# Optimization experiments

Measured on AMD Instinct MI355X. Metric: run time of the kernel, lower is better.

The kernel has to match this reference:

```python
import jax, jax.numpy as jnp
from jax import lax
import numpy as np

B, N = 64, 128           # graphs per batch, nodes per graph
MAX_LEVEL = 3
N_TRUNKS, TRUNK_LEN = 32, 32
H, OUT = 256, 10


def setup_inputs() -> dict:
    key = jax.random.key(0)
    ks = jax.random.split(key, 12)
    batch_feature = jax.random.normal(ks[0], (B, N), dtype=jnp.float32)
    trunk_idx = jax.random.randint(ks[1], (MAX_LEVEL, N_TRUNKS, TRUNK_LEN), 0, N, dtype=jnp.int32)
    trunk_len = jax.random.randint(ks[2], (MAX_LEVEL, N_TRUNKS), 1, TRUNK_LEN + 1, dtype=jnp.int32)
    s = 1.0 / np.sqrt(H)
    W_enc = jax.random.uniform(ks[3], (1, H), jnp.float32, -1.0, 1.0)
    b_enc = jax.random.uniform(ks[4], (H,), jnp.float32, -1.0, 1.0)
    W_ih = jax.random.uniform(ks[5], (MAX_LEVEL, 4 * H, H), jnp.float32, -s, s)
    W_hh = jax.random.uniform(ks[6], (MAX_LEVEL, 4 * H, H), jnp.float32, -s, s)
    b_ih = jax.random.uniform(ks[7], (MAX_LEVEL, 4 * H), jnp.float32, -s, s)
    b_hh = jax.random.uniform(ks[8], (MAX_LEVEL, 4 * H), jnp.float32, -s, s)
    W_lin = jax.random.uniform(ks[9], (MAX_LEVEL, H, OUT), jnp.float32, -s, s)
    b_lin = jax.random.uniform(ks[10], (MAX_LEVEL, OUT), jnp.float32, -s, s)
    return {"batch_feature": batch_feature, "trunk_idx": trunk_idx, "trunk_len": trunk_len,
            "W_enc": W_enc, "b_enc": b_enc, "W_ih": W_ih, "W_hh": W_hh,
            "b_ih": b_ih, "b_hh": b_hh, "W_lin": W_lin, "b_lin": b_lin}


def _lstm_scan(seq, W_ih, W_hh, b):
    """seq: [L, M, H] -> all hidden states [L, M, H] (single-layer LSTM, PyTorch gate order i,f,g,o)."""
    M = seq.shape[1]
    Hd = W_hh.shape[1]
    def step(carry, x_t):
        h, c = carry
        gates = x_t @ W_ih.T + h @ W_hh.T + b   # [M, 4H]
        i, f, g, o = jnp.split(gates, 4, axis=-1)
        c = jax.nn.sigmoid(f) * c + jax.nn.sigmoid(i) * jnp.tanh(g)
        h = jax.nn.sigmoid(o) * jnp.tanh(c)
        return (h, c), h
    init = (jnp.zeros((M, Hd), seq.dtype), jnp.zeros((M, Hd), seq.dtype))
    _, hs = lax.scan(step, init, seq)
    return hs


def reference(batch_feature, trunk_idx, trunk_len, W_enc, b_enc, W_ih, W_hh, b_ih, b_hh, W_lin, b_lin):
    Bv, Nv = batch_feature.shape
    Hd = W_enc.shape[1]
    # node encoder on scalar features: x [B*N, 1] @ W_enc [1, H]
    x_attr = (batch_feature.reshape(-1, 1) @ W_enc + b_enc).reshape(Bv, Nv, Hd)
    trunk_len = jnp.maximum(trunk_len, 1)
    score = jnp.zeros((Bv, W_lin.shape[-1]), x_attr.dtype)
    for l in range(trunk_idx.shape[0]):
        idx = trunk_idx[l]                       # [T, L]
        T, L = idx.shape
        seqs = x_attr[:, idx]                    # gather trunks -> [B, T, L, H]
        seqs = seqs.reshape(Bv * T, L, Hd).transpose(1, 0, 2)   # [L, B*T, H]
        hs = _lstm_scan(seqs, W_ih[l], W_hh[l], b_ih[l] + b_hh[l])  # [L, B*T, H]
        lens = jnp.tile(trunk_len[l], Bv)        # [B*T]
        h_last = hs[lens - 1, jnp.arange(Bv * T)]   # hidden at last valid step (== packed h_n)
        h_trunk = h_last.reshape(Bv, T, Hd).sum(axis=1)  # scatter-sum per graph (indices are i repeated T times)
        score = score + h_trunk @ W_lin[l] + b_lin[l]
    return score


if __name__ == "__main__":
    out = reference(**setup_inputs())
    print(out.shape, out.dtype)
```

## Files before the change

kernel.cpp:

```cpp
#include <hip/hip_runtime.h>
#include <hip/hip_bf16.h>
#include <stdint.h>

#define B_   64
#define N_   128
#define H_   256
#define FH   1024
#define NT   32
#define TL   32
#define LV   3
#define OUT_ 10
#define NTRK 96
#define UNITS 384

typedef __attribute__((ext_vector_type(4))) int   int4v;
typedef __attribute__((ext_vector_type(4))) float f32x4;

#define QW  (0.0625f / 127.0f)
#define QH  (1.0f / 127.0f)
#define QS  (QW * QH)
#define L2E 1.442695041f
#define QSI (-L2E * QS)
#define QSG (2.0f * L2E * QS)
#define C2  (2.0f * L2E)

__device__ inline float exp2f_(float x) { return __builtin_amdgcn_exp2f(x); }
__device__ inline float rcpf_(float x)  { return __builtin_amdgcn_rcpf(x); }

__global__ void prep_all(const float* __restrict__ W_enc, const float* __restrict__ b_enc,
                         const float* __restrict__ W_ih, const float* __restrict__ b_ih,
                         const float* __restrict__ b_hh, const float* __restrict__ W_hh,
                         const float* __restrict__ b_lin, const int* __restrict__ trunk_len,
                         float* __restrict__ u, float* __restrict__ v,
                         char* __restrict__ whh_i8, float* __restrict__ out,
                         int* __restrict__ sorted, int* __restrict__ counter) {
    int blk = blockIdx.x;
    int tid = threadIdx.x;
    if (blk < 768) {
        int j = blk * 4 + (tid >> 6);
        int lane = tid & 63;
        const float4 w  = ((const float4*)(W_ih + (size_t)j * H_))[lane];
        const float4 we = ((const float4*)W_enc)[lane];
        const float4 be = ((const float4*)b_enc)[lane];
        float du = w.x * we.x + w.y * we.y + w.z * we.z + w.w * we.w;
        float dv = w.x * be.x + w.y * be.y + w.z * be.z + w.w * be.w;
        for (int m = 32; m >= 1; m >>= 1) { du += __shfl_xor(du, m); dv += __shfl_xor(dv, m); }
        if (lane == 0) {
            int g = (j & 1023) >> 8;
            float s = (g == 2) ? (2.0f * L2E) : (-L2E);
            u[j] = s * du;
            v[j] = s * (dv + b_ih[j] + b_hh[j]);
        }
    } else if (blk < 1536) {
        int gid = (blk - 768) * 256 + tid;
        const float4 w = ((const float4*)W_hh)[gid];
        char4 o;
        int a0 = __float2int_rn(w.x * (127.0f / 0.0625f));
        int a1 = __float2int_rn(w.y * (127.0f / 0.0625f));
        int a2 = __float2int_rn(w.z * (127.0f / 0.0625f));
        int a3 = __float2int_rn(w.w * (127.0f / 0.0625f));
        a0 = a0 > 127 ? 127 : (a0 < -127 ? -127 : a0);
        a1 = a1 > 127 ? 127 : (a1 < -127 ? -127 : a1);
        a2 = a2 > 127 ? 127 : (a2 < -127 ? -127 : a2);
        a3 = a3 > 127 ? 127 : (a3 < -127 ? -127 : a3);
        o.x = (char)a0; o.y = (char)a1; o.z = (char)a2; o.w = (char)a3;
        ((char4*)whh_i8)[gid] = o;
        if (gid < B_ * OUT_) {
            int oo = gid % OUT_;
            out[gid] = b_lin[oo] + b_lin[OUT_ + oo] + b_lin[2 * OUT_ + oo];
        }
    } else {
        if (tid < NTRK) {
            int li = trunk_len[tid]; if (li < 1) li = 1;
            int rank = 0;
            for (int j2 = 0; j2 < NTRK; ++j2) {
                int lj = trunk_len[j2]; if (lj < 1) lj = 1;
                rank += (lj > li) || (lj == li && j2 < tid);
            }
            sorted[rank] = tid;
        }
        if (tid == 0) *counter = 0;
    }
}

__global__ __launch_bounds__(1024) __attribute__((amdgpu_waves_per_eu(4, 4)))
void lstm_main(const float* __restrict__ bfeat, const int* __restrict__ trunk_idx,
               const int* __restrict__ trunk_len,
               const char* __restrict__ whh_i8,
               const float* __restrict__ u, const float* __restrict__ v,
               const float* __restrict__ W_lin, const int* __restrict__ sorted,
               int* __restrict__ counter, float* __restrict__ out) {
    __shared__ __align__(16) char hbuf[2][16][272];
    __shared__ __align__(16) float sbuf[2][16];
    __shared__ int sh_uid;

    const int tid = threadIdx.x;
    const int w = tid >> 6;
    const int lane = tid & 63;
    const int col = lane & 15;
    const int q = lane >> 4;

    int4v z4; z4[0] = 0; z4[1] = 0; z4[2] = 0; z4[3] = 0;
    asm volatile("" : "+v"(z4));

    for (;;) {
        if (tid == 0) sh_uid = atomicAdd(counter, 1);
        __syncthreads();
        const int uid = sh_uid;
        if (uid >= UNITS) break;

        const int r = uid >> 2, qq = uid & 3;
        const int tt = sorted[r];
        const int l = tt >> 5;
        const int b0 = qq * 16;

        int len = trunk_len[tt];
        if (len < 1) len = 1;
        const int* tix = trunk_idx + tt * TL;
        const char* whh_l = whh_i8 + (size_t)l * FH * H_;

        int4v Breg[4][4];
        #pragma unroll
        for (int g = 0; g < 4; ++g) {
            int j = g * 256 + w * 16 + col;
            const char* bp = whh_l + (size_t)j * H_ + q * 16;
            #pragma unroll
            for (int k = 0; k < 4; ++k)
                Breg[g][k] = *(const int4v*)(bp + k * 64);
        }

        float u_r[4], v_r[4];
        {
            const float* u_l = u + l * FH;
            const float* v_l = v + l * FH;
            #pragma unroll
            for (int g = 0; g < 4; ++g) {
                int j = g * 256 + w * 16 + col;
                u_r[g] = u_l[j];
                v_r[g] = v_l[j];
            }
        }

        float c_r[4];

        if (tid < 16) sbuf[0][tid] = bfeat[(b0 + tid) * N_ + tix[0]];
        __syncthreads();

        {
            if (len > 1 && tid < 16) sbuf[1][tid] = bfeat[(b0 + tid) * N_ + tix[1]];
            f32x4 sv = *(const f32x4*)&sbuf[0][q * 4];
            #pragma unroll
            for (int rg = 0; rg < 4; ++rg) {
                float xi = fmaf(sv[rg], u_r[0], v_r[0]);
                float xg = fmaf(sv[rg], u_r[2], v_r[2]);
                float xo = fmaf(sv[rg], u_r[3], v_r[3]);
                float si = rcpf_(exp2f_(xi) + 1.0f);
                float so = rcpf_(exp2f_(xo) + 1.0f);
                float tg = fmaf(-2.0f, rcpf_(exp2f_(xg) + 1.0f), 1.0f);
                float cn = si * tg;
                c_r[rg] = cn;
                float th127 = fmaf(-254.0f, rcpf_(exp2f_(C2 * cn) + 1.0f), 127.0f);
                hbuf[1][q * 4 + rg][w * 16 + col] = (char)__float2int_rn(so * th127);
            }
            __syncthreads();
        }

        for (int p = 1; p < len; ++p) {
            const int ri = p & 1, wi = ri ^ 1;

            if (p + 1 < len && tid < 16)
                sbuf[wi][tid] = bfeat[(b0 + tid) * N_ + tix[p + 1]];

            int4v a_f[4];
            #pragma unroll
            for (int k = 0; k < 4; ++k)
                a_f[k] = *(const int4v*)&hbuf[ri][col][k * 64 + q * 16];

            f32x4 sv = *(const f32x4*)&sbuf[ri][q * 4];

            int4v acc[4];
            #pragma unroll
            for (int g = 0; g < 4; ++g) {
                acc[g] = __builtin_amdgcn_mfma_i32_16x16x64_i8(a_f[0], Breg[g][0], z4, 0, 0, 0);
                #pragma unroll
                for (int k = 1; k < 4; ++k)
                    acc[g] = __builtin_amdgcn_mfma_i32_16x16x64_i8(a_f[k], Breg[g][k], acc[g], 0, 0, 0);
            }

            #pragma unroll
            for (int rg = 0; rg < 4; ++rg) {
                float xi = fmaf((float)acc[0][rg], QSI, fmaf(sv[rg], u_r[0], v_r[0]));
                float xf = fmaf((float)acc[1][rg], QSI, fmaf(sv[rg], u_r[1], v_r[1]));
                float xg = fmaf((float)acc[2][rg], QSG, fmaf(sv[rg], u_r[2], v_r[2]));
                float xo = fmaf((float)acc[3][rg], QSI, fmaf(sv[rg], u_r[3], v_r[3]));
                float si = rcpf_(exp2f_(xi) + 1.0f);
                float sf = rcpf_(exp2f_(xf) + 1.0f);
                float so = rcpf_(exp2f_(xo) + 1.0f);
                float tg = fmaf(-2.0f, rcpf_(exp2f_(xg) + 1.0f), 1.0f);
                float cn = fmaf(sf, c_r[rg], si * tg);
                c_r[rg] = cn;
                float th127 = fmaf(-254.0f, rcpf_(exp2f_(C2 * cn) + 1.0f), 127.0f);
                hbuf[wi][q * 4 + rg][w * 16 + col] = (char)__float2int_rn(so * th127);
            }

            __syncthreads();
        }

        const char (*hl)[272] = hbuf[len & 1];
        const float* wl = W_lin + l * H_ * OUT_;
        if (tid < 16 * OUT_) {
            int m = tid / OUT_, o = tid % OUT_;
            float s = 0.f;
            for (int k = 0; k < H_; ++k)
                s += (float)hl[m][k] * QH * wl[k * OUT_ + o];
            atomicAdd(&out[(b0 + m) * OUT_ + o], s);
        }
    }
}

extern "C" void kernel_launch(void* const* d_in, const int* in_sizes, int n_in,
                              void* d_out, int out_size, void* d_ws, size_t ws_size,
                              hipStream_t stream) {
    const float* bfeat = (const float*)d_in[0];
    const int*   tidx  = (const int*)d_in[1];
    const int*   tlen  = (const int*)d_in[2];
    const float* W_enc = (const float*)d_in[3];
    const float* b_enc = (const float*)d_in[4];
    const float* W_ih  = (const float*)d_in[5];
    const float* W_hh  = (const float*)d_in[6];
    const float* b_ih  = (const float*)d_in[7];
    const float* b_hh  = (const float*)d_in[8];
    const float* W_lin = (const float*)d_in[9];
    const float* b_lin = (const float*)d_in[10];
    float* out = (float*)d_out;

    char*  whh_i8 = (char*)d_ws;
    float* u = (float*)((char*)d_ws + 786432);
    float* v = (float*)((char*)d_ws + 786432 + 12288);
    int* sorted  = (int*)((char*)d_ws + 811008);
    int* counter = (int*)((char*)d_ws + 811392);

    prep_all<<<1537, 256, 0, stream>>>(W_enc, b_enc, W_ih, b_ih, b_hh, W_hh, b_lin,
                                       tlen, u, v, whh_i8, out, sorted, counter);
    lstm_main<<<256, 1024, 0, stream>>>(bfeat, tidx, tlen, whh_i8, u, v, W_lin,
                                        sorted, counter, out);
}
```

Before: 146.5 us.

## Halve block size to 512 threads with two column tiles per wave, launch 512 blocks

Measured after the change: 327.1 us. +123.3%, slower.

```diff
diff --git a/kernel.cpp b/kernel.cpp
--- a/kernel.cpp
+++ b/kernel.cpp
@@ -12,6 +12,7 @@
 #define OUT_ 10
 #define NTRK 96
 #define UNITS 384
+#define NWORK 512
 
 typedef __attribute__((ext_vector_type(4))) int   int4v;
 typedef __attribute__((ext_vector_type(4))) float f32x4;
@@ -83,7 +84,7 @@
     }
 }
 
-__global__ __launch_bounds__(1024) __attribute__((amdgpu_waves_per_eu(4, 4)))
+__global__ __launch_bounds__(512) __attribute__((amdgpu_waves_per_eu(4, 4)))
 void lstm_main(const float* __restrict__ bfeat, const int* __restrict__ trunk_idx,
                const int* __restrict__ trunk_len,
                const char* __restrict__ whh_i8,
@@ -119,29 +120,33 @@
         const int* tix = trunk_idx + tt * TL;
         const char* whh_l = whh_i8 + (size_t)l * FH * H_;
 
-        int4v Breg[4][4];
+        int4v Breg[4][2][4];
         #pragma unroll
-        for (int g = 0; g < 4; ++g) {
-            int j = g * 256 + w * 16 + col;
-            const char* bp = whh_l + (size_t)j * H_ + q * 16;
-            #pragma unroll
-            for (int k = 0; k < 4; ++k)
-                Breg[g][k] = *(const int4v*)(bp + k * 64);
-        }
-
-        float u_r[4], v_r[4];
+        for (int g = 0; g < 4; ++g)
+            #pragma unroll
+            for (int n = 0; n < 2; ++n) {
+                int j = g * 256 + w * 32 + n * 16 + col;
+                const char* bp = whh_l + (size_t)j * H_ + q * 16;
+                #pragma unroll
+                for (int k = 0; k < 4; ++k)
+                    Breg[g][n][k] = *(const int4v*)(bp + k * 64);
+            }
+
+        float u_r[4][2], v_r[4][2];
         {
             const float* u_l = u + l * FH;
             const float* v_l = v + l * FH;
             #pragma unroll
-            for (int g = 0; g < 4; ++g) {
-                int j = g * 256 + w * 16 + col;
-                u_r[g] = u_l[j];
-                v_r[g] = v_l[j];
-            }
-        }
-
-        float c_r[4];
+            for (int g = 0; g < 4; ++g)
+                #pragma unroll
+                for (int n = 0; n < 2; ++n) {
+                    int j = g * 256 + w * 32 + n * 16 + col;
+                    u_r[g][n] = u_l[j];
+                    v_r[g][n] = v_l[j];
+                }
+        }
+
+        float c_r[2][4];
 
         if (tid < 16) sbuf[0][tid] = bfeat[(b0 + tid) * N_ + tix[0]];
         __syncthreads();
@@ -150,18 +155,21 @@
             if (len > 1 && tid < 16) sbuf[1][tid] = bfeat[(b0 + tid) * N_ + tix[1]];
             f32x4 sv = *(const f32x4*)&sbuf[0][q * 4];
             #pragma unroll
-            for (int rg = 0; rg < 4; ++rg) {
-                float xi = fmaf(sv[rg], u_r[0], v_r[0]);
-                float xg = fmaf(sv[rg], u_r[2], v_r[2]);
-                float xo = fmaf(sv[rg], u_r[3], v_r[3]);
-                float si = rcpf_(exp2f_(xi) + 1.0f);
-                float so = rcpf_(exp2f_(xo) + 1.0f);
-                float tg = fmaf(-2.0f, rcpf_(exp2f_(xg) + 1.0f), 1.0f);
-                float cn = si * tg;
-                c_r[rg] = cn;
-                float th127 = fmaf(-254.0f, rcpf_(exp2f_(C2 * cn) + 1.0f), 127.0f);
-                hbuf[1][q * 4 + rg][w * 16 + col] = (char)__float2int_rn(so * th127);
-            }
+            for (int n = 0; n < 2; ++n)
+                #pragma unroll
+                for (int rg = 0; rg < 4; ++rg) {
+                    float xi = fmaf(sv[rg], u_r[0][n], v_r[0][n]);
+                    float xg = fmaf(sv[rg], u_r[2][n], v_r[2][n]);
+                    float xo = fmaf(sv[rg], u_r[3][n], v_r[3][n]);
+                    float si = rcpf_(exp2f_(xi) + 1.0f);
+                    float so = rcpf_(exp2f_(xo) + 1.0f);
+                    float tg = fmaf(-2.0f, rcpf_(exp2f_(xg) + 1.0f), 1.0f);
+                    float cn = si * tg;
+                    c_r[n][rg] = cn;
+                    float th127 = fmaf(-254.0f, rcpf_(exp2f_(C2 * cn) + 1.0f), 127.0f);
+                    hbuf[1][q * 4 + rg][w * 32 + n * 16 + col] =
+                        (char)__float2int_rn(so * th127);
+                }
             __syncthreads();
         }
 
@@ -178,29 +186,33 @@
 
             f32x4 sv = *(const f32x4*)&sbuf[ri][q * 4];
 
-            int4v acc[4];
-            #pragma unroll
-            for (int g = 0; g < 4; ++g) {
-                acc[g] = __builtin_amdgcn_mfma_i32_16x16x64_i8(a_f[0], Breg[g][0], z4, 0, 0, 0);
-                #pragma unroll
-                for (int k = 1; k < 4; ++k)
-                    acc[g] = __builtin_amdgcn_mfma_i32_16x16x64_i8(a_f[k], Breg[g][k], acc[g], 0, 0, 0);
-            }
-
-            #pragma unroll
-            for (int rg = 0; rg < 4; ++rg) {
-                float xi = fmaf((float)acc[0][rg], QSI, fmaf(sv[rg], u_r[0], v_r[0]));
-                float xf = fmaf((float)acc[1][rg], QSI, fmaf(sv[rg], u_r[1], v_r[1]));
-                float xg = fmaf((float)acc[2][rg], QSG, fmaf(sv[rg], u_r[2], v_r[2]));
-                float xo = fmaf((float)acc[3][rg], QSI, fmaf(sv[rg], u_r[3], v_r[3]));
-                float si = rcpf_(exp2f_(xi) + 1.0f);
-                float sf = rcpf_(exp2f_(xf) + 1.0f);
-                float so = rcpf_(exp2f_(xo) + 1.0f);
-                float tg = fmaf(-2.0f, rcpf_(exp2f_(xg) + 1.0f), 1.0f);
-                float cn = fmaf(sf, c_r[rg], si * tg);
-                c_r[rg] = cn;
-                float th127 = fmaf(-254.0f, rcpf_(exp2f_(C2 * cn) + 1.0f), 127.0f);
-                hbuf[wi][q * 4 + rg][w * 16 + col] = (char)__float2int_rn(so * th127);
+            #pragma unroll
+            for (int n = 0; n < 2; ++n) {
+                int4v acc[4];
+                #pragma unroll
+                for (int g = 0; g < 4; ++g) {
+                    acc[g] = __builtin_amdgcn_mfma_i32_16x16x64_i8(a_f[0], Breg[g][n][0], z4, 0, 0, 0);
+                    #pragma unroll
+                    for (int k = 1; k < 4; ++k)
+                        acc[g] = __builtin_amdgcn_mfma_i32_16x16x64_i8(a_f[k], Breg[g][n][k], acc[g], 0, 0, 0);
+                }
+
+                #pragma unroll
+                for (int rg = 0; rg < 4; ++rg) {
+                    float xi = fmaf((float)acc[0][rg], QSI, fmaf(sv[rg], u_r[0][n], v_r[0][n]));
+                    float xf = fmaf((float)acc[1][rg], QSI, fmaf(sv[rg], u_r[1][n], v_r[1][n]));
+                    float xg = fmaf((float)acc[2][rg], QSG, fmaf(sv[rg], u_r[2][n], v_r[2][n]));
+                    float xo = fmaf((float)acc[3][rg], QSI, fmaf(sv[rg], u_r[3][n], v_r[3][n]));
+                    float si = rcpf_(exp2f_(xi) + 1.0f);
+                    float sf = rcpf_(exp2f_(xf) + 1.0f);
+                    float so = rcpf_(exp2f_(xo) + 1.0f);
+                    float tg = fmaf(-2.0f, rcpf_(exp2f_(xg) + 1.0f), 1.0f);
+                    float cn = fmaf(sf, c_r[n][rg], si * tg);
+                    c_r[n][rg] = cn;
+                    float th127 = fmaf(-254.0f, rcpf_(exp2f_(C2 * cn) + 1.0f), 127.0f);
+                    hbuf[wi][q * 4 + rg][w * 32 + n * 16 + col] =
+                        (char)__float2int_rn(so * th127);
+                }
             }
 
             __syncthreads();
@@ -242,6 +254,6 @@
 
     prep_all<<<1537, 256, 0, stream>>>(W_enc, b_enc, W_ih, b_ih, b_hh, W_hh, b_lin,
                                        tlen, u, v, whh_i8, out, sorted, counter);
-    lstm_main<<<256, 1024, 0, stream>>>(bfeat, tidx, tlen, whh_i8, u, v, W_lin,
-                                        sorted, counter, out);
+    lstm_main<<<NWORK, 512, 0, stream>>>(bfeat, tidx, tlen, whh_i8, u, v, W_lin,
+                                         sorted, counter, out);
 }
```
